# Optimization experiments

Measured on AMD Instinct MI355X. Metric: run time of the kernel, lower is better.

## Reference

```python
import jax, jax.numpy as jnp
import numpy as np

N = 32768      # total nodes
G = 64         # graphs
NPG = 512      # nodes per graph (equal-size graphs)
K = 256        # ceil(NPG * pooling_ratio), pooling_ratio=0.5
D = 256        # input_dim
H = 256        # hidden_dim
FD = 3 * H     # fusion dim
C = 10         # num_classes
E = 262144     # edges
EPS = 1e-5     # BatchNorm eps


def setup_inputs() -> dict:
    key = jax.random.key(0)
    ks = jax.random.split(key, 20)
    w = lambda k, s: jax.random.normal(k, s, jnp.float32) * 0.05
    inp = {
        'x': jax.random.normal(ks[0], (N, D), jnp.float32),
        'edge_index': jax.random.randint(ks[1], (2, E), 0, N, jnp.int64),
        'batch': (jnp.arange(N, dtype=jnp.int64) // NPG),
        'w_s1': w(ks[2], (D, H)), 'b_s1': jnp.zeros((H,), jnp.float32),
        'w_s21': w(ks[3], (D, H)), 'b_s21': jnp.zeros((H,), jnp.float32),
        'w_s22': w(ks[4], (H, H)), 'b_s22': jnp.zeros((H,), jnp.float32),
        'w_raw': w(ks[5], (D, H)), 'b_raw': jnp.zeros((H,), jnp.float32),
        'w_pos': w(ks[6], (FD, 1)), 'b_pos': jnp.zeros((1,), jnp.float32),
        'w_neg': w(ks[7], (FD, 1)), 'b_neg': jnp.zeros((1,), jnp.float32),
        'w_pool': w(ks[8], (FD, FD)), 'b_pool': jnp.zeros((FD,), jnp.float32),
        'w1': w(ks[9], (2 * FD, 256)), 'b1': jnp.zeros((256,), jnp.float32),
        'g1': jnp.ones((256,), jnp.float32), 'be1': jnp.zeros((256,), jnp.float32),
        'w2': w(ks[10], (256, 256)), 'b2': jnp.zeros((256,), jnp.float32),
        'g2': jnp.ones((256,), jnp.float32), 'be2': jnp.zeros((256,), jnp.float32),
        'w3': w(ks[11], (256, 256)), 'b3': jnp.zeros((256,), jnp.float32),
        'g3': jnp.ones((256,), jnp.float32), 'be3': jnp.zeros((256,), jnp.float32),
        'w4': w(ks[12], (256, C)), 'b4': jnp.zeros((C,), jnp.float32),
    }
    return inp


def _gcn(x, W, b, src, dst, dinv):
    # PyG GCNConv: linear, then sym-normalized aggregation with self-loops
    h = x @ W
    norm = dinv[src] * dinv[dst]
    agg = jax.ops.segment_sum(h[src] * norm[:, None], dst, num_segments=N)
    agg = agg + h * (dinv * dinv)[:, None]  # self-loop contribution
    return agg + b


def _bn(z, g, b):
    m = z.mean(0)
    v = z.var(0)  # biased, as torch BN training-mode normalization
    return (z - m) * jax.lax.rsqrt(v + EPS) * g + b


def _mlp(z, w1, b1, g1, be1, w2, b2, g2, be2, w3, b3, g3, be3, w4, b4):
    z = jax.nn.relu(_bn(z @ w1 + b1, g1, be1))  # dropout=identity (eval)
    idt = z
    o = jax.nn.relu(_bn(z @ w2 + b2, g2, be2))
    z = o + idt
    idt = z
    o = jax.nn.relu(_bn(z @ w3 + b3, g3, be3))
    z = o + idt
    return z @ w4 + b4


def _topk_mask(scores):
    # equal-size graphs -> per-graph top-k via one batched lax.top_k
    sg = scores.reshape(G, NPG)
    _, idx = jax.lax.top_k(sg, K)
    mask = jnp.zeros((G, NPG), bool).at[jnp.arange(G)[:, None], idx].set(True)
    return mask.reshape(-1)


def _readout(xt, mask):
    m = mask[:, None]
    xs = jnp.where(m, xt, 0.0).reshape(G, NPG, FD)
    mean_pool = xs.sum(1) / K
    mx = jnp.where(m, xt, -jnp.inf).reshape(G, NPG, FD).max(1)
    return jnp.concatenate([mean_pool, mx], axis=1)


def reference(x, edge_index, batch, w_s1, b_s1, w_s21, b_s21, w_s22, b_s22,
              w_raw, b_raw, w_pos, b_pos, w_neg, b_neg, w_pool, b_pool,
              w1, b1, g1, be1, w2, b2, g2, be2, w3, b3, g3, be3, w4, b4):
    src, dst = edge_index[0], edge_index[1]
    deg = jax.ops.segment_sum(jnp.ones_like(src, jnp.float32), dst, num_segments=N) + 1.0
    dinv = jax.lax.rsqrt(deg)
    lrelu = lambda z: jax.nn.leaky_relu(z, 0.01)

    h_s1 = lrelu(_gcn(x, w_s1, b_s1, src, dst, dinv))
    h_s2 = lrelu(_gcn(lrelu(_gcn(x, w_s21, b_s21, src, dst, dinv)), w_s22, b_s22, src, dst, dinv))
    h_raw = x @ w_raw + b_raw
    h_final = jnp.concatenate([h_s1, h_s2, h_raw], axis=1)  # [N, FD]

    score_pos = jax.nn.sigmoid(_gcn(h_final, w_pos, b_pos, src, dst, dinv)).reshape(-1)
    score_neg = jax.nn.sigmoid(_gcn(h_final, w_neg, b_neg, src, dst, dinv)).reshape(-1)

    xt = jax.nn.sigmoid(h_final @ w_pool + b_pool)  # pool_transform for all nodes; mask selects
    mask_pos = _topk_mask(score_pos)
    mask_neg = _topk_mask(score_neg)

    mlp = lambda e: _mlp(e, w1, b1, g1, be1, w2, b2, g2, be2, w3, b3, g3, be3, w4, b4)
    logits_pos = mlp(_readout(xt, mask_pos))
    probs_pos = jax.nn.softmax(logits_pos, axis=1)
    logits_neg = mlp(_readout(xt, mask_neg))
    probs_neg = jax.nn.softmax(logits_neg, axis=1)
    return (logits_pos, probs_pos, probs_neg, score_pos, score_neg, batch)
```

## Files before the change

kernel.cpp:

```cpp
#include <hip/hip_runtime.h>
#include <hip/hip_bf16.h>

#define N_NODES 32768
#define NGRAPH  64
#define NPG     512
#define TOPK    256
#define HID     256
#define FDIM    768
#define NEDGE   262144
#define NCLS    10
#define BN_EPS  1e-5f

#define IN_BF16 0
#define OUT_BF16 0

typedef __attribute__((ext_vector_type(8))) short short8;
typedef __attribute__((ext_vector_type(4))) float f32x4;

__device__ __forceinline__ float bf2f(unsigned short u) {
    return __uint_as_float(((unsigned)u) << 16);
}
__device__ __forceinline__ unsigned short f2bf(float f) {
    unsigned x = __float_as_uint(f);
    unsigned r = (x + 0x7fffu + ((x >> 16) & 1u)) >> 16;
    return (unsigned short)r;
}
__device__ __forceinline__ float in_ld(const void* p, size_t i) {
#if IN_BF16
    return bf2f(((const unsigned short*)p)[i]);
#else
    return ((const float*)p)[i];
#endif
}
__device__ __forceinline__ void st_out(void* o, size_t i, float v) {
#if OUT_BF16
    ((unsigned short*)o)[i] = f2bf(v);
#else
    ((float*)o)[i] = v;
#endif
}

__device__ __forceinline__ void async_cp16(const unsigned short* g, unsigned short* l) {
    __builtin_amdgcn_global_load_lds(
        (const __attribute__((address_space(1))) unsigned int*)g,
        (__attribute__((address_space(3))) unsigned int*)l, 16, 0, 0);
}

__global__ __launch_bounds__(256) void cvt_kernel(const float* __restrict__ in,
                                                  unsigned short* __restrict__ out, int n) {
    int i = blockIdx.x * 256 + threadIdx.x;
    if (i < n) out[i] = f2bf(in[i]);
}

__global__ __launch_bounds__(256) void cvt_t_kernel(const float* __restrict__ in,
                                                    unsigned short* __restrict__ out, int K, int N) {
    __shared__ unsigned short tile[32][33];
    int bk = blockIdx.x * 32, bn = blockIdx.y * 32;
    int tx = threadIdx.x & 31, ty = threadIdx.x >> 5;
#pragma unroll
    for (int i = 0; i < 32; i += 8)
        tile[ty + i][tx] = f2bf(in[(size_t)(bk + ty + i) * N + bn + tx]);
    __syncthreads();
#pragma unroll
    for (int i = 0; i < 32; i += 8)
        out[(size_t)(bn + ty + i) * K + bk + tx] = tile[tx][ty + i];
}

__global__ __launch_bounds__(256) void detect_kernel(const int* __restrict__ eb, int* __restrict__ flag) {
    int i = blockIdx.x * 256 + threadIdx.x;
    int v = eb[2 * (size_t)i + 1];
    unsigned long long b = __ballot(v != 0);
    if ((threadIdx.x & 63) == 0 && b)
        atomicAdd(flag, (int)__popcll(b));
}

__global__ __launch_bounds__(256) void hist_kernel(const int* __restrict__ eb, const int* __restrict__ flag,
                                                   int* __restrict__ deg) {
    int e = blockIdx.x * 256 + threadIdx.x;
    int st = (*flag == 0) ? 2 : 1;
    unsigned d = ((const unsigned*)eb)[(size_t)(NEDGE + e) * st] & (N_NODES - 1);
    atomicAdd(&deg[d], 1);
}

__global__ __launch_bounds__(256) void dinv_kernel(const int* __restrict__ deg, float* __restrict__ dinv) {
    int i = blockIdx.x * 256 + threadIdx.x;
    dinv[i] = rsqrtf((float)deg[i] + 1.0f);
}

__global__ __launch_bounds__(1024) void scan_kernel(const int* __restrict__ cnt, int* __restrict__ rowptr,
                                                    int* __restrict__ cursor) {
    __shared__ int part[1024];
    int t = threadIdx.x;
    int base = t * 32;
    int loc[32];
    int s = 0;
#pragma unroll
    for (int i = 0; i < 32; i++) { loc[i] = cnt[base + i]; s += loc[i]; }
    part[t] = s;
    __syncthreads();
    for (int off = 1; off < 1024; off <<= 1) {
        int v = (t >= off) ? part[t - off] : 0;
        __syncthreads();
        part[t] += v;
        __syncthreads();
    }
    int run = (t == 0) ? 0 : part[t - 1];
#pragma unroll
    for (int i = 0; i < 32; i++) {
        rowptr[base + i] = run;
        cursor[base + i] = run;
        run += loc[i];
    }
    if (t == 1023) rowptr[N_NODES] = run;
}

__global__ __launch_bounds__(256) void scatter_kernel(const int* __restrict__ eb, const int* __restrict__ flag,
                                                      int* __restrict__ cursor, int* __restrict__ srcs) {
    int e = blockIdx.x * 256 + threadIdx.x;
    int st = (*flag == 0) ? 2 : 1;
    unsigned s = ((const unsigned*)eb)[(size_t)e * st] & (N_NODES - 1);
    unsigned d = ((const unsigned*)eb)[(size_t)(NEDGE + e) * st] & (N_NODES - 1);
    int p = atomicAdd(&cursor[d], 1);
    srcs[p] = (int)s;
}

__global__ __launch_bounds__(256) void gemm_kernel(const unsigned short* __restrict__ A,
                                                   const unsigned short* __restrict__ WT,
                                                   const float* __restrict__ bias,
                                                   unsigned short* __restrict__ C,
                                                   int K, int Nn, int ldC, int colOff, int epi) {
    __shared__ unsigned short As[128 * 64];
    __shared__ unsigned short Bs[128 * 64];
    const int tid = threadIdx.x;
    const int wave = tid >> 6;
    const int lane = tid & 63;
    const int bm = blockIdx.y * 128;
    const int bn = blockIdx.x * 128;
    const int wm = (wave >> 1) * 64;
    const int wn = (wave & 1) * 64;
    const int l15 = lane & 15;
    const int q = lane >> 4;

    f32x4 acc[4][4] = {};

    const int srow = lane >> 3;
    const int schunk = lane & 7;

    for (int k0 = 0; k0 < K; k0 += 64) {
        __syncthreads();
#pragma unroll
        for (int t = 0; t < 4; t++) {
            int r = t * 32 + wave * 8 + srow;
            int gc = schunk ^ (r & 7);
            const unsigned short* ga = A + (size_t)(bm + r) * K + k0 + gc * 8;
            const unsigned short* gb = WT + (size_t)(bn + r) * K + k0 + gc * 8;
            unsigned short* la = &As[(t * 32 + wave * 8) * 64];
            unsigned short* lb = &Bs[(t * 32 + wave * 8) * 64];
            async_cp16(ga, la);
            async_cp16(gb, lb);
        }
        __syncthreads();

#pragma unroll
        for (int h = 0; h < 2; h++) {
            short8 af[4], bfv[4];
            int p = (h * 4 + q) ^ (l15 & 7);
#pragma unroll
            for (int t = 0; t < 4; t++) {
                int m = wm + t * 16 + l15;
                int n = wn + t * 16 + l15;
                af[t] = *(const short8*)&As[m * 64 + p * 8];
                bfv[t] = *(const short8*)&Bs[n * 64 + p * 8];
            }
#pragma unroll
            for (int tm = 0; tm < 4; tm++)
#pragma unroll
                for (int tn = 0; tn < 4; tn++)
                    acc[tm][tn] = __builtin_amdgcn_mfma_f32_16x16x32_bf16(af[tm], bfv[tn], acc[tm][tn], 0, 0, 0);
        }
    }

#pragma unroll
    for (int tm = 0; tm < 4; tm++) {
        int row = bm + wm + tm * 16 + q * 4;
#pragma unroll
        for (int tn = 0; tn < 4; tn++) {
            int col = bn + wn + tn * 16 + l15;
            float bv = bias ? bias[col] : 0.0f;
#pragma unroll
            for (int r = 0; r < 4; r++) {
                float v = acc[tm][tn][r] + bv;
                if (epi == 1) v = 1.0f / (1.0f + __expf(-v));
                C[(size_t)(row + r) * ldC + colOff + col] = f2bf(v);
            }
        }
    }
}

__global__ __launch_bounds__(256) void agg_kernel(const unsigned short* __restrict__ h,
                                                  const int* __restrict__ rowptr, const int* __restrict__ srcs,
                                                  const float* __restrict__ dinv, const void* __restrict__ bias,
                                                  unsigned short* __restrict__ out, int ldOut, int colOff,
                                                  int do_lrelu) {
    int wave = threadIdx.x >> 6, lane = threadIdx.x & 63;
    int v = blockIdx.x * 4 + wave;
    int f0 = lane * 4;
    float a0 = 0.f, a1 = 0.f, a2 = 0.f, a3 = 0.f;
    int s = rowptr[v], e = rowptr[v + 1];
    for (int i = s; i < e; i++) {
        int u = srcs[i] & (N_NODES - 1);
        float du = dinv[u];
        uint2 hv = *(const uint2*)(h + (size_t)u * 256 + f0);
        a0 += bf2f((unsigned short)(hv.x & 0xffff)) * du;
        a1 += bf2f((unsigned short)(hv.x >> 16)) * du;
        a2 += bf2f((unsigned short)(hv.y & 0xffff)) * du;
        a3 += bf2f((unsigned short)(hv.y >> 16)) * du;
    }
    float dv = dinv[v], dv2 = dv * dv;
    uint2 sv = *(const uint2*)(h + (size_t)v * 256 + f0);
    float r0 = dv * a0 + bf2f((unsigned short)(sv.x & 0xffff)) * dv2 + in_ld(bias, f0 + 0);
    float r1 = dv * a1 + bf2f((unsigned short)(sv.x >> 16)) * dv2 + in_ld(bias, f0 + 1);
    float r2 = dv * a2 + bf2f((unsigned short)(sv.y & 0xffff)) * dv2 + in_ld(bias, f0 + 2);
    float r3 = dv * a3 + bf2f((unsigned short)(sv.y >> 16)) * dv2 + in_ld(bias, f0 + 3);
    if (do_lrelu) {
        r0 = r0 > 0.f ? r0 : 0.01f * r0;
        r1 = r1 > 0.f ? r1 : 0.01f * r1;
        r2 = r2 > 0.f ? r2 : 0.01f * r2;
        r3 = r3 > 0.f ? r3 : 0.01f * r3;
    }
    unsigned o0 = f2bf(r0), o1 = f2bf(r1), o2 = f2bf(r2), o3 = f2bf(r3);
    uint2 ov = make_uint2((o1 << 16) | o0, (o3 << 16) | o2);
    *(uint2*)(out + (size_t)v * ldOut + colOff + f0) = ov;
}

__global__ __launch_bounds__(256) void score_mv_kernel(const unsigned short* __restrict__ hf,
                                                       const void* __restrict__ wp, const void* __restrict__ wn,
                                                       float* __restrict__ svp, float* __restrict__ svn) {
    int wave = threadIdx.x >> 6, lane = threadIdx.x & 63;
    int v = blockIdx.x * 4 + wave;
    float sp = 0.f, sn = 0.f;
#pragma unroll
    for (int i = 0; i < 3; i++) {
        int k = i * 256 + lane * 4;
        uint2 hv = *(const uint2*)(hf + (size_t)v * 768 + k);
        float x0 = bf2f((unsigned short)(hv.x & 0xffff));
        float x1 = bf2f((unsigned short)(hv.x >> 16));
        float x2 = bf2f((unsigned short)(hv.y & 0xffff));
        float x3 = bf2f((unsigned short)(hv.y >> 16));
        sp += x0 * in_ld(wp, k) + x1 * in_ld(wp, k + 1) + x2 * in_ld(wp, k + 2) + x3 * in_ld(wp, k + 3);
        sn += x0 * in_ld(wn, k) + x1 * in_ld(wn, k + 1) + x2 * in_ld(wn, k + 2) + x3 * in_ld(wn, k + 3);
    }
    for (int off = 32; off >= 1; off >>= 1) {
        sp += __shfl_down(sp, off, 64);
        sn += __shfl_down(sn, off, 64);
    }
    if (lane == 0) { svp[v] = sp; svn[v] = sn; }
}

__global__ __launch_bounds__(256) void score_agg_kernel(const float* __restrict__ svp, const float* __restrict__ svn,
                                                        const int* __restrict__ rowptr, const int* __restrict__ srcs,
                                                        const float* __restrict__ dinv,
                                                        const void* __restrict__ bp, const void* __restrict__ bn_,
                                                        float* __restrict__ scp, float* __restrict__ scn,
                                                        void* __restrict__ dout) {
    int v = blockIdx.x * 256 + threadIdx.x;
    float ap = 0.f, an = 0.f;
    int s = rowptr[v], e = rowptr[v + 1];
    for (int i = s; i < e; i++) {
        int u = srcs[i] & (N_NODES - 1);
        float du = dinv[u];
        ap += svp[u] * du;
        an += svn[u] * du;
    }
    float dv = dinv[v], dv2 = dv * dv;
    float zp = dv * ap + svp[v] * dv2 + in_ld(bp, 0);
    float zn = dv * an + svn[v] * dv2 + in_ld(bn_, 0);
    float pp = 1.0f / (1.0f + __expf(-zp));
    float pn = 1.0f / (1.0f + __expf(-zn));
    scp[v] = pp;
    scn[v] = pn;
    st_out(dout, 1920 + (size_t)v, pp);
    st_out(dout, 1920 + (size_t)N_NODES + v, pn);
}

__global__ __launch_bounds__(512) void topk_kernel(const float* __restrict__ sc, unsigned char* __restrict__ mask) {
    __shared__ float s[512];
    int g = blockIdx.x, i = threadIdx.x;
    float my = sc[(size_t)g * 512 + i];
    s[i] = my;
    __syncthreads();
    int cnt = 0;
    for (int j = 0; j < 512; j++) {
        float o = s[j];
        cnt += (int)((o > my) || ((o == my) && (j < i)));
    }
    mask[(size_t)g * 512 + i] = (cnt < TOPK) ? 1 : 0;
}

__global__ __launch_bounds__(256) void readout2_kernel(const unsigned short* __restrict__ xt,
                                                       const unsigned char* __restrict__ maskp,
                                                       const unsigned char* __restrict__ maskn,
                                                       float* __restrict__ eout) {
    int g = blockIdx.x;
    int c = blockIdx.y;
    int wv = threadIdx.x >> 6, lane = threadIdx.x & 63;
    int f = c * 64 + lane;
    __shared__ unsigned char mp[512], mn[512];
    __shared__ float red[4][64][4];
    for (int i = threadIdx.x; i < 512; i += 256) {
        mp[i] = maskp[(size_t)g * 512 + i];
        mn[i] = maskn[(size_t)g * 512 + i];
    }
    __syncthreads();
    float sp = 0.f, sn = 0.f, xp = -INFINITY, xn = -INFINITY;
    const unsigned short* base = xt + ((size_t)g * 512 + wv * 128) * 768 + f;
    for (int v = 0; v < 128; v++) {
        float x = bf2f(base[(size_t)v * 768]);
        if (mp[wv * 128 + v]) { sp += x; xp = fmaxf(xp, x); }
        if (mn[wv * 128 + v]) { sn += x; xn = fmaxf(xn, x); }
    }
    red[wv][lane][0] = sp; red[wv][lane][1] = xp;
    red[wv][lane][2] = sn; red[wv][lane][3] = xn;
    __syncthreads();
    if (wv == 0) {
#pragma unroll
        for (int w = 1; w < 4; w++) {
            sp += red[w][lane][0]; xp = fmaxf(xp, red[w][lane][1]);
            sn += red[w][lane][2]; xn = fmaxf(xn, red[w][lane][3]);
        }
        float* erp = eout + (size_t)g * 1536;
        float* ern = eout + (size_t)(64 + g) * 1536;
        erp[f] = sp * (1.0f / TOPK);
        erp[768 + f] = xp;
        ern[f] = sn * (1.0f / TOPK);
        ern[768 + f] = xn;
    }
}

__global__ __launch_bounds__(256) void mlp_gemm2_kernel(const float* __restrict__ in,
                                                        const float* __restrict__ W,
                                                        const float* __restrict__ b,
                                                        float* __restrict__ out, int K) {
    __shared__ float row[1536];
    __shared__ float red[4][64];
    int r = blockIdx.x, cg = blockIdx.y;
    int wv = threadIdx.x >> 6, lane = threadIdx.x & 63;
    int c = cg * 64 + lane;
    for (int k = threadIdx.x; k < K; k += 256) row[k] = in[(size_t)r * K + k];
    __syncthreads();
    int kpw = K >> 2;
    const float* wp = W + (size_t)(wv * kpw) * 256 + c;
    const float* rp = row + wv * kpw;
    float acc = 0.f;
#pragma unroll 4
    for (int k = 0; k < kpw; k++)
        acc += rp[k] * wp[(size_t)k * 256];
    red[wv][lane] = acc;
    __syncthreads();
    if (wv == 0) {
        float v = red[0][lane] + red[1][lane] + red[2][lane] + red[3][lane] + b[c];
        out[(size_t)r * 256 + c] = v;
    }
}

__global__ __launch_bounds__(64) void bn_kernel(const float* __restrict__ z, const void* __restrict__ gamma,
                                                const void* __restrict__ beta, const float* __restrict__ res,
                                                float* __restrict__ out) {
    int f = blockIdx.x & 255, g = blockIdx.x >> 8, r = threadIdx.x;
    size_t idx = (size_t)(g * 64 + r) * 256 + f;
    float x = z[idx];
    float s = x, sq = x * x;
    for (int off = 1; off < 64; off <<= 1) {
        s += __shfl_xor(s, off, 64);
        sq += __shfl_xor(sq, off, 64);
    }
    float m = s * (1.0f / 64.0f);
    float var = sq * (1.0f / 64.0f) - m * m;
    float y = (x - m) * rsqrtf(var + BN_EPS) * in_ld(gamma, f) + in_ld(beta, f);
    y = fmaxf(y, 0.0f);
    if (res) y += res[idx];
    out[idx] = y;
}

__global__ __launch_bounds__(64) void logits_kernel(const float* __restrict__ act, const void* __restrict__ w4,
                                                    const void* __restrict__ b4, float* __restrict__ lg) {
    int idx = blockIdx.x * 64 + threadIdx.x;
    if (idx >= 128 * NCLS) return;
    int r = idx / NCLS, c = idx % NCLS;
    float acc = in_ld(b4, c);
    for (int k = 0; k < 256; k++) acc += act[(size_t)r * 256 + k] * in_ld(w4, (size_t)k * NCLS + c);
    lg[idx] = acc;
}

__global__ __launch_bounds__(64) void softmax_kernel(const float* __restrict__ lg, void* __restrict__ dout) {
    int r = blockIdx.x * 64 + threadIdx.x;
    if (r >= 128) return;
    float l[NCLS];
    float mx = -1e30f;
    for (int c = 0; c < NCLS; c++) { l[c] = lg[(size_t)r * NCLS + c]; mx = fmaxf(mx, l[c]); }
    float sum = 0.f;
    float ex[NCLS];
    for (int c = 0; c < NCLS; c++) { ex[c] = __expf(l[c] - mx); sum += ex[c]; }
    float inv = 1.0f / sum;
    int g = r >> 6, rr = r & 63;
    if (g == 0) {
        for (int c = 0; c < NCLS; c++) st_out(dout, (size_t)rr * NCLS + c, l[c]);
        for (int c = 0; c < NCLS; c++) st_out(dout, 640 + (size_t)rr * NCLS + c, ex[c] * inv);
    } else {
        for (int c = 0; c < NCLS; c++) st_out(dout, 1280 + (size_t)rr * NCLS + c, ex[c] * inv);
    }
}

__global__ __launch_bounds__(256) void batch_kernel(void* __restrict__ dout) {
    int i = blockIdx.x * 256 + threadIdx.x;
    st_out(dout, 1920 + 2 * (size_t)N_NODES + i, (float)(i >> 9));
}

extern "C" void kernel_launch(void* const* d_in, const int* in_sizes, int n_in,
                              void* d_out, int out_size, void* d_ws, size_t ws_size,
                              hipStream_t stream) {
    (void)in_sizes; (void)n_in; (void)out_size; (void)ws_size;

    const float* x = (const float*)d_in[0];
    const int* eb = (const int*)d_in[1];
    const float* w_s1 = (const float*)d_in[3];
    const float* b_s1 = (const float*)d_in[4];
    const float* w_s21 = (const float*)d_in[5];
    const float* b_s21 = (const float*)d_in[6];
    const float* w_s22 = (const float*)d_in[7];
    const float* b_s22 = (const float*)d_in[8];
    const float* w_raw = (const float*)d_in[9];
    const float* b_raw = (const float*)d_in[10];
    const void* w_pos = d_in[11];
    const void* b_pos = d_in[12];
    const void* w_neg = d_in[13];
    const void* b_neg = d_in[14];
    const float* w_pool = (const float*)d_in[15];
    const float* b_pool = (const float*)d_in[16];
    const float* w1 = (const float*)d_in[17];  const float* b1 = (const float*)d_in[18];
    const void* g1 = d_in[19];  const void* be1 = d_in[20];
    const float* w2 = (const float*)d_in[21];  const float* b2 = (const float*)d_in[22];
    const void* g2 = d_in[23];  const void* be2 = d_in[24];
    const float* w3 = (const float*)d_in[25];  const float* b3 = (const float*)d_in[26];
    const void* g3 = d_in[27];  const void* be3 = d_in[28];
    const void* w4 = d_in[29];  const void* b4 = d_in[30];

    char* ws = (char*)d_ws;
    size_t off = 0;
    auto alloc = [&](size_t b) -> void* {
        void* p = ws + off;
        off += (b + 255) & ~(size_t)255;
        return p;
    };
    int* flag = (int*)alloc(256);
    int* deg = (int*)alloc((size_t)N_NODES * 4);
    float* dinv = (float*)alloc((size_t)N_NODES * 4);
    int* rowptr = (int*)alloc((size_t)(N_NODES + 1) * 4);
    int* cursor = (int*)alloc((size_t)N_NODES * 4);
    int* srcs = (int*)alloc((size_t)NEDGE * 4);
    unsigned short* xbf = (unsigned short*)alloc((size_t)N_NODES * 256 * 2);
    unsigned short* wb_s1 = (unsigned short*)alloc((size_t)256 * 256 * 2);
    unsigned short* wb_s21 = (unsigned short*)alloc((size_t)256 * 256 * 2);
    unsigned short* wb_s22 = (unsigned short*)alloc((size_t)256 * 256 * 2);
    unsigned short* wb_raw = (unsigned short*)alloc((size_t)256 * 256 * 2);
    unsigned short* wb_pool = (unsigned short*)alloc((size_t)768 * 768 * 2);
    unsigned short* tmpA = (unsigned short*)alloc((size_t)N_NODES * 256 * 2);
    unsigned short* tmpB = (unsigned short*)alloc((size_t)N_NODES * 256 * 2);
    unsigned short* hfin = (unsigned short*)alloc((size_t)N_NODES * 768 * 2);
    unsigned short* xt = (unsigned short*)alloc((size_t)N_NODES * 768 * 2);
    float* svp = (float*)alloc((size_t)N_NODES * 4);
    float* svn = (float*)alloc((size_t)N_NODES * 4);
    float* scp = (float*)alloc((size_t)N_NODES * 4);
    float* scn = (float*)alloc((size_t)N_NODES * 4);
    unsigned char* maskp = (unsigned char*)alloc(N_NODES);
    unsigned char* maskn = (unsigned char*)alloc(N_NODES);
    float* ebuf = (float*)alloc((size_t)128 * 1536 * 4);
    float* zb = (float*)alloc((size_t)128 * 256 * 4);
    float* act1 = (float*)alloc((size_t)128 * 256 * 4);
    float* act2 = (float*)alloc((size_t)128 * 256 * 4);
    float* act3 = (float*)alloc((size_t)128 * 256 * 4);
    float* lg = (float*)alloc((size_t)128 * NCLS * 4);

    hipMemsetAsync(flag, 0, 256, stream);
    hipMemsetAsync(deg, 0, (size_t)N_NODES * 4, stream);
    detect_kernel<<<NEDGE / 256, 256, 0, stream>>>(eb, flag);
    hist_kernel<<<NEDGE / 256, 256, 0, stream>>>(eb, flag, deg);
    dinv_kernel<<<N_NODES / 256, 256, 0, stream>>>(deg, dinv);
    scan_kernel<<<1, 1024, 0, stream>>>(deg, rowptr, cursor);
    scatter_kernel<<<NEDGE / 256, 256, 0, stream>>>(eb, flag, cursor, srcs);

    cvt_kernel<<<(N_NODES * 256 + 255) / 256, 256, 0, stream>>>(x, xbf, N_NODES * 256);
    {
        dim3 g8(8, 8), g24(24, 24);
        cvt_t_kernel<<<g8, 256, 0, stream>>>(w_s1, wb_s1, 256, 256);
        cvt_t_kernel<<<g8, 256, 0, stream>>>(w_s21, wb_s21, 256, 256);
        cvt_t_kernel<<<g8, 256, 0, stream>>>(w_s22, wb_s22, 256, 256);
        cvt_t_kernel<<<g8, 256, 0, stream>>>(w_raw, wb_raw, 256, 256);
        cvt_t_kernel<<<g24, 256, 0, stream>>>(w_pool, wb_pool, 768, 768);
    }

    dim3 gA(256 / 128, N_NODES / 128);
    dim3 gP(768 / 128, N_NODES / 128);

    gemm_kernel<<<gA, 256, 0, stream>>>(xbf, wb_s1, nullptr, tmpA, 256, 256, 256, 0, 0);
    agg_kernel<<<N_NODES / 4, 256, 0, stream>>>(tmpA, rowptr, srcs, dinv, b_s1, hfin, 768, 0, 1);
    gemm_kernel<<<gA, 256, 0, stream>>>(xbf, wb_s21, nullptr, tmpA, 256, 256, 256, 0, 0);
    agg_kernel<<<N_NODES / 4, 256, 0, stream>>>(tmpA, rowptr, srcs, dinv, b_s21, tmpB, 256, 0, 1);
    gemm_kernel<<<gA, 256, 0, stream>>>(tmpB, wb_s22, nullptr, tmpA, 256, 256, 256, 0, 0);
    agg_kernel<<<N_NODES / 4, 256, 0, stream>>>(tmpA, rowptr, srcs, dinv, b_s22, hfin, 768, 256, 1);
    gemm_kernel<<<gA, 256, 0, stream>>>(xbf, wb_raw, b_raw, hfin, 256, 256, 768, 512, 0);
    gemm_kernel<<<gP, 256, 0, stream>>>(hfin, wb_pool, b_pool, xt, 768, 768, 768, 0, 1);
    score_mv_kernel<<<N_NODES / 4, 256, 0, stream>>>(hfin, w_pos, w_neg, svp, svn);
    score_agg_kernel<<<N_NODES / 256, 256, 0, stream>>>(svp, svn, rowptr, srcs, dinv, b_pos, b_neg, scp, scn, d_out);
    topk_kernel<<<NGRAPH, 512, 0, stream>>>(scp, maskp);
    topk_kernel<<<NGRAPH, 512, 0, stream>>>(scn, maskn);
    {
        dim3 gR(NGRAPH, FDIM / 64);
        readout2_kernel<<<gR, 256, 0, stream>>>(xt, maskp, maskn, ebuf);
    }
    {
        dim3 gM(128, 4);
        mlp_gemm2_kernel<<<gM, 256, 0, stream>>>(ebuf, w1, b1, zb, 1536);
        bn_kernel<<<512, 64, 0, stream>>>(zb, g1, be1, nullptr, act1);
        mlp_gemm2_kernel<<<gM, 256, 0, stream>>>(act1, w2, b2, zb, 256);
        bn_kernel<<<512, 64, 0, stream>>>(zb, g2, be2, act1, act2);
        mlp_gemm2_kernel<<<gM, 256, 0, stream>>>(act2, w3, b3, zb, 256);
        bn_kernel<<<512, 64, 0, stream>>>(zb, g3, be3, act2, act3);
    }
    logits_kernel<<<(128 * NCLS + 63) / 64, 64, 0, stream>>>(act3, w4, b4, lg);
    softmax_kernel<<<2, 64, 0, stream>>>(lg, d_out);
    batch_kernel<<<N_NODES / 256, 256, 0, stream>>>(d_out);
}
```

Measured before the change: 647.7 us.

## Fuse three x-based GEMMs into one concatenated-weight GEMM with XCD tile swizzle

Concatenates the transposed w_s1, w_s21 and w_raw weights into one 768-wide matrix so the three GEMMs that read x run as a single launch. Its epilogue routes column ranges to two temporaries and to the raw slice of hfin. A block-index swizzle also remaps tiles so neighbouring row tiles land on the same XCD, aiming for better L2 reuse of A. The intent is to read x once instead of three times and cut launch overhead, at the cost of one extra temporary buffer.

```diff
diff --git a/kernel.cpp b/kernel.cpp
--- a/kernel.cpp
+++ b/kernel.cpp
@@ -46,6 +46,15 @@
         (__attribute__((address_space(3))) unsigned int*)l, 16, 0, 0);
 }
 
+__device__ __forceinline__ void tile_swizzle(int& bm, int& bn) {
+    int nx = gridDim.x;
+    int L = blockIdx.y * nx + blockIdx.x;
+    int xcd = L & 7;
+    int j = L >> 3;
+    bm = ((j / nx) * 8 + xcd) * 128;
+    bn = (j % nx) * 128;
+}
+
 __global__ __launch_bounds__(256) void cvt_kernel(const float* __restrict__ in,
                                                   unsigned short* __restrict__ out, int n) {
     int i = blockIdx.x * 256 + threadIdx.x;
@@ -124,62 +133,60 @@
     srcs[p] = (int)s;
 }
 
+#define GEMM_CORE(K_)                                                           \
+    __shared__ unsigned short As[128 * 64];                                     \
+    __shared__ unsigned short Bs[128 * 64];                                     \
+    const int tid = threadIdx.x;                                                \
+    const int wave = tid >> 6;                                                  \
+    const int lane = tid & 63;                                                  \
+    int bm, bn;                                                                 \
+    tile_swizzle(bm, bn);                                                       \
+    const int wm = (wave >> 1) * 64;                                            \
+    const int wn = (wave & 1) * 64;                                             \
+    const int l15 = lane & 15;                                                  \
+    const int q = lane >> 4;                                                    \
+    f32x4 acc[4][4] = {};                                                       \
+    const int srow = lane >> 3;                                                 \
+    const int schunk = lane & 7;                                                \
+    for (int k0 = 0; k0 < (K_); k0 += 64) {                                     \
+        __syncthreads();                                                        \
+        _Pragma("unroll")                                                       \
+        for (int t = 0; t < 4; t++) {                                           \
+            int r = t * 32 + wave * 8 + srow;                                   \
+            int gc = schunk ^ (r & 7);                                          \
+            const unsigned short* ga = A + (size_t)(bm + r) * (K_) + k0 + gc * 8;\
+            const unsigned short* gb = WT + (size_t)(bn + r) * (K_) + k0 + gc * 8;\
+            unsigned short* la = &As[(t * 32 + wave * 8) * 64];                 \
+            unsigned short* lb = &Bs[(t * 32 + wave * 8) * 64];                 \
+            async_cp16(ga, la);                                                 \
+            async_cp16(gb, lb);                                                 \
+        }                                                                       \
+        __syncthreads();                                                        \
+        _Pragma("unroll")                                                       \
+        for (int h = 0; h < 2; h++) {                                           \
+            short8 af[4], bfv[4];                                               \
+            int p = (h * 4 + q) ^ (l15 & 7);                                    \
+            _Pragma("unroll")                                                   \
+            for (int t = 0; t < 4; t++) {                                       \
+                int m = wm + t * 16 + l15;                                      \
+                int n = wn + t * 16 + l15;                                      \
+                af[t] = *(const short8*)&As[m * 64 + p * 8];                    \
+                bfv[t] = *(const short8*)&Bs[n * 64 + p * 8];                   \
+            }                                                                   \
+            _Pragma("unroll")                                                   \
+            for (int tm = 0; tm < 4; tm++)                                      \
+                _Pragma("unroll")                                               \
+                for (int tn = 0; tn < 4; tn++)                                  \
+                    acc[tm][tn] = __builtin_amdgcn_mfma_f32_16x16x32_bf16(af[tm], bfv[tn], acc[tm][tn], 0, 0, 0); \
+        }                                                                       \
+    }
+
 __global__ __launch_bounds__(256) void gemm_kernel(const unsigned short* __restrict__ A,
                                                    const unsigned short* __restrict__ WT,
                                                    const float* __restrict__ bias,
                                                    unsigned short* __restrict__ C,
-                                                   int K, int Nn, int ldC, int colOff, int epi) {
-    __shared__ unsigned short As[128 * 64];
-    __shared__ unsigned short Bs[128 * 64];
-    const int tid = threadIdx.x;
-    const int wave = tid >> 6;
-    const int lane = tid & 63;
-    const int bm = blockIdx.y * 128;
-    const int bn = blockIdx.x * 128;
-    const int wm = (wave >> 1) * 64;
-    const int wn = (wave & 1) * 64;
-    const int l15 = lane & 15;
-    const int q = lane >> 4;
-
-    f32x4 acc[4][4] = {};
-
-    const int srow = lane >> 3;
-    const int schunk = lane & 7;
-
-    for (int k0 = 0; k0 < K; k0 += 64) {
-        __syncthreads();
-#pragma unroll
-        for (int t = 0; t < 4; t++) {
-            int r = t * 32 + wave * 8 + srow;
-            int gc = schunk ^ (r & 7);
-            const unsigned short* ga = A + (size_t)(bm + r) * K + k0 + gc * 8;
-            const unsigned short* gb = WT + (size_t)(bn + r) * K + k0 + gc * 8;
-            unsigned short* la = &As[(t * 32 + wave * 8) * 64];
-            unsigned short* lb = &Bs[(t * 32 + wave * 8) * 64];
-            async_cp16(ga, la);
-            async_cp16(gb, lb);
-        }
-        __syncthreads();
-
-#pragma unroll
-        for (int h = 0; h < 2; h++) {
-            short8 af[4], bfv[4];
-            int p = (h * 4 + q) ^ (l15 & 7);
-#pragma unroll
-            for (int t = 0; t < 4; t++) {
-                int m = wm + t * 16 + l15;
-                int n = wn + t * 16 + l15;
-                af[t] = *(const short8*)&As[m * 64 + p * 8];
-                bfv[t] = *(const short8*)&Bs[n * 64 + p * 8];
-            }
-#pragma unroll
-            for (int tm = 0; tm < 4; tm++)
-#pragma unroll
-                for (int tn = 0; tn < 4; tn++)
-                    acc[tm][tn] = __builtin_amdgcn_mfma_f32_16x16x32_bf16(af[tm], bfv[tn], acc[tm][tn], 0, 0, 0);
-        }
-    }
-
+                                                   int K, int ldC, int colOff, int epi) {
+    GEMM_CORE(K)
 #pragma unroll
     for (int tm = 0; tm < 4; tm++) {
         int row = bm + wm + tm * 16 + q * 4;
@@ -192,6 +199,37 @@
                 float v = acc[tm][tn][r] + bv;
                 if (epi == 1) v = 1.0f / (1.0f + __expf(-v));
                 C[(size_t)(row + r) * ldC + colOff + col] = f2bf(v);
+            }
+        }
+    }
+}
+
+__global__ __launch_bounds__(256) void gemm3_kernel(const unsigned short* __restrict__ A,
+                                                    const unsigned short* __restrict__ WT,
+                                                    const float* __restrict__ b_raw,
+                                                    unsigned short* __restrict__ tA,
+                                                    unsigned short* __restrict__ tB,
+                                                    unsigned short* __restrict__ hfin) {
+    GEMM_CORE(256)
+#pragma unroll
+    for (int tm = 0; tm < 4; tm++) {
+        int row = bm + wm + tm * 16 + q * 4;
+#pragma unroll
+        for (int tn = 0; tn < 4; tn++) {
+            int col = bn + wn + tn * 16 + l15;
+            if (col < 256) {
+#pragma unroll
+                for (int r = 0; r < 4; r++)
+                    tA[(size_t)(row + r) * 256 + col] = f2bf(acc[tm][tn][r]);
+            } else if (col < 512) {
+#pragma unroll
+                for (int r = 0; r < 4; r++)
+                    tB[(size_t)(row + r) * 256 + (col - 256)] = f2bf(acc[tm][tn][r]);
+            } else {
+                float bv = b_raw[col - 512];
+#pragma unroll
+                for (int r = 0; r < 4; r++)
+                    hfin[(size_t)(row + r) * 768 + col] = f2bf(acc[tm][tn][r] + bv);
             }
         }
     }
@@ -459,12 +497,11 @@
     int* cursor = (int*)alloc((size_t)N_NODES * 4);
     int* srcs = (int*)alloc((size_t)NEDGE * 4);
     unsigned short* xbf = (unsigned short*)alloc((size_t)N_NODES * 256 * 2);
-    unsigned short* wb_s1 = (unsigned short*)alloc((size_t)256 * 256 * 2);
-    unsigned short* wb_s21 = (unsigned short*)alloc((size_t)256 * 256 * 2);
+    unsigned short* wcat = (unsigned short*)alloc((size_t)768 * 256 * 2);
     unsigned short* wb_s22 = (unsigned short*)alloc((size_t)256 * 256 * 2);
-    unsigned short* wb_raw = (unsigned short*)alloc((size_t)256 * 256 * 2);
     unsigned short* wb_pool = (unsigned short*)alloc((size_t)768 * 768 * 2);
-    unsigned short* tmpA = (unsigned short*)alloc((size_t)N_NODES * 256 * 2);
+    unsigned short* tA = (unsigned short*)alloc((size_t)N_NODES * 256 * 2);
+    unsigned short* tB = (unsigned short*)alloc((size_t)N_NODES * 256 * 2);
     unsigned short* tmpB = (unsigned short*)alloc((size_t)N_NODES * 256 * 2);
     unsigned short* hfin = (unsigned short*)alloc((size_t)N_NODES * 768 * 2);
     unsigned short* xt = (unsigned short*)alloc((size_t)N_NODES * 768 * 2);
@@ -492,24 +529,23 @@
     cvt_kernel<<<(N_NODES * 256 + 255) / 256, 256, 0, stream>>>(x, xbf, N_NODES * 256);
     {
         dim3 g8(8, 8), g24(24, 24);
-        cvt_t_kernel<<<g8, 256, 0, stream>>>(w_s1, wb_s1, 256, 256);
-        cvt_t_kernel<<<g8, 256, 0, stream>>>(w_s21, wb_s21, 256, 256);
+        cvt_t_kernel<<<g8, 256, 0, stream>>>(w_s1, wcat, 256, 256);
+        cvt_t_kernel<<<g8, 256, 0, stream>>>(w_s21, wcat + (size_t)256 * 256, 256, 256);
+        cvt_t_kernel<<<g8, 256, 0, stream>>>(w_raw, wcat + (size_t)512 * 256, 256, 256);
         cvt_t_kernel<<<g8, 256, 0, stream>>>(w_s22, wb_s22, 256, 256);
-        cvt_t_kernel<<<g8, 256, 0, stream>>>(w_raw, wb_raw, 256, 256);
         cvt_t_kernel<<<g24, 256, 0, stream>>>(w_pool, wb_pool, 768, 768);
     }
 
+    dim3 gG3(768 / 128, N_NODES / 128);
     dim3 gA(256 / 128, N_NODES / 128);
     dim3 gP(768 / 128, N_NODES / 128);
 
-    gemm_kernel<<<gA, 256, 0, stream>>>(xbf, wb_s1, nullptr, tmpA, 256, 256, 256, 0, 0);
-    agg_kernel<<<N_NODES / 4, 256, 0, stream>>>(tmpA, rowptr, srcs, dinv, b_s1, hfin, 768, 0, 1);
-    gemm_kernel<<<gA, 256, 0, stream>>>(xbf, wb_s21, nullptr, tmpA, 256, 256, 256, 0, 0);
-    agg_kernel<<<N_NODES / 4, 256, 0, stream>>>(tmpA, rowptr, srcs, dinv, b_s21, tmpB, 256, 0, 1);
-    gemm_kernel<<<gA, 256, 0, stream>>>(tmpB, wb_s22, nullptr, tmpA, 256, 256, 256, 0, 0);
-    agg_kernel<<<N_NODES / 4, 256, 0, stream>>>(tmpA, rowptr, srcs, dinv, b_s22, hfin, 768, 256, 1);
-    gemm_kernel<<<gA, 256, 0, stream>>>(xbf, wb_raw, b_raw, hfin, 256, 256, 768, 512, 0);
-    gemm_kernel<<<gP, 256, 0, stream>>>(hfin, wb_pool, b_pool, xt, 768, 768, 768, 0, 1);
+    gemm3_kernel<<<gG3, 256, 0, stream>>>(xbf, wcat, b_raw, tA, tB, hfin);
+    agg_kernel<<<N_NODES / 4, 256, 0, stream>>>(tA, rowptr, srcs, dinv, b_s1, hfin, 768, 0, 1);
+    agg_kernel<<<N_NODES / 4, 256, 0, stream>>>(tB, rowptr, srcs, dinv, b_s21, tmpB, 256, 0, 1);
+    gemm_kernel<<<gA, 256, 0, stream>>>(tmpB, wb_s22, nullptr, tA, 256, 256, 0, 0);
+    agg_kernel<<<N_NODES / 4, 256, 0, stream>>>(tA, rowptr, srcs, dinv, b_s22, hfin, 768, 256, 1);
+    gemm_kernel<<<gP, 256, 0, stream>>>(hfin, wb_pool, b_pool, xt, 768, 768, 0, 1);
     score_mv_kernel<<<N_NODES / 4, 256, 0, stream>>>(hfin, w_pos, w_neg, svp, svn);
     score_agg_kernel<<<N_NODES / 256, 256, 0, stream>>>(svp, svn, rowptr, srcs, dinv, b_pos, b_neg, scp, scn, d_out);
     topk_kernel<<<NGRAPH, 512, 0, stream>>>(scp, maskp);
```

Result: faster. 627.4 us (-3.1%).
